# Optimization experiments

Hardware: AMD Instinct MI355X
Metric: run time of the kernel (lower is better)

## Reference

```python
import jax, jax.numpy as jnp
import numpy as np

B, D, H = 4096, 256, 1024
TRACE_STEPS = 10
T_FINAL = 1.0


def setup_inputs() -> dict:
    key = jax.random.key(0)
    k0, k1, k2 = jax.random.split(key, 3)
    s1 = 1.0 / np.sqrt(D + 1)
    s2 = 1.0 / np.sqrt(H)
    return {
        "x": jax.random.normal(k0, (B, D), dtype=jnp.float32),
        "W1": jax.random.uniform(k1, (D + 1, H), jnp.float32, -s1, s1),
        "b1": jnp.zeros((H,), jnp.float32),
        "W2": jax.random.uniform(k2, (H, D), jnp.float32, -s2, s2),
        "b2": jnp.zeros((D,), jnp.float32),
    }


def _odefun(params, t, z):
    # FFJORD vector field: tanh MLP on [z, t]. z: [B, D] -> [B, D]
    W1, b1, W2, b2 = params
    tcol = jnp.full((z.shape[0], 1), t, dtype=z.dtype)
    h = jnp.tanh(jnp.concatenate([z, tcol], axis=-1) @ W1 + b1)
    return h @ W2 + b2


def _rademacher(key, shape, dtype):
    # randint(0,2)*2-1, matching the torch probe construction
    return jax.random.randint(key, shape, 0, 2).astype(dtype) * 2.0 - 1.0


def _aug_dynamics(params, t, state, e):
    # state: [B, D+1] = [z | logp]; e: [TRACE_STEPS, B, D] Rademacher probes.
    # torch computes etf = grad((f*e).sum(), z) = e^T J, div = (e^T J)*e summed.
    # e^T J e == e . (J e), so forward-mode jvp gives identical math.
    z = state[:, :-1]
    f = lambda zz: _odefun(params, t, zz)

    def probe(ei):
        f_z, Je = jax.jvp(f, (z,), (ei,))
        return f_z, jnp.sum(Je * ei, axis=-1)  # [B]

    f_z, divs = jax.vmap(probe)(e)
    f_z = f_z[0]                       # primal identical across probes
    div_est = jnp.mean(divs, axis=0)   # average of trace_steps estimates
    return jnp.concatenate([f_z, -div_est[:, None]], axis=-1)


def reference(x, W1, b1, W2, b2):
    params = (W1, b1, W2, b2)
    Bx = x.shape[0]
    ekey = jax.random.key(42)
    probes = lambda i: _rademacher(jax.random.fold_in(ekey, i), (TRACE_STEPS, Bx, D), x.dtype)

    # initial augmented state: [z, logp=0]
    y0 = jnp.concatenate([x, jnp.zeros((Bx, 1), x.dtype)], axis=-1)

    # t_grid = [0, T] with 2 points -> fixed-grid rk4 takes ONE RK4 step of size T
    h = T_FINAL
    g = lambda t, y, i: _aug_dynamics(params, t, y, probes(i))
    k1 = g(0.0, y0, 0)
    k2 = g(0.5 * h, y0 + 0.5 * h * k1, 1)
    k3 = g(0.5 * h, y0 + 0.5 * h * k2, 2)
    k4 = g(h, y0 + h * k3, 3)
    y1 = y0 + (h / 6.0) * (k1 + 2.0 * k2 + 2.0 * k3 + k4)

    # module returns the full trajectory `output`: [len(t_grid), B, D+1]
    return jnp.stack([y0, y1], axis=0)
```

## Files before the change

### kernel.cpp

```cpp
#include <hip/hip_runtime.h>
#include <stdint.h>

#define BATCH 4096
#define DIMD  256
#define DIMH  1024
#define EPAD  264
#define NEPW  163840

typedef __attribute__((ext_vector_type(8))) short short8;
typedef __attribute__((ext_vector_type(4))) float float4v;

struct Keys4 { uint32_t a[4]; uint32_t b[4]; };

__host__ __device__ static inline uint32_t rotl32(uint32_t v, int r) {
    return (v << r) | (v >> (32 - r));
}

__host__ __device__ static inline void tf2x32(uint32_t k0, uint32_t k1,
                                              uint32_t c0, uint32_t c1,
                                              uint32_t& o0, uint32_t& o1) {
    uint32_t ks0 = k0, ks1 = k1, ks2 = k0 ^ k1 ^ 0x1BD11BDAu;
    uint32_t x0 = c0 + ks0, x1 = c1 + ks1;
#define TF_R4(a, b, c, d)                                   \
    x0 += x1; x1 = rotl32(x1, a); x1 ^= x0;                 \
    x0 += x1; x1 = rotl32(x1, b); x1 ^= x0;                 \
    x0 += x1; x1 = rotl32(x1, c); x1 ^= x0;                 \
    x0 += x1; x1 = rotl32(x1, d); x1 ^= x0;
    TF_R4(13, 15, 26, 6)  x0 += ks1; x1 += ks2 + 1u;
    TF_R4(17, 29, 16, 24) x0 += ks2; x1 += ks0 + 2u;
    TF_R4(13, 15, 26, 6)  x0 += ks0; x1 += ks1 + 3u;
    TF_R4(17, 29, 16, 24) x0 += ks1; x1 += ks2 + 4u;
    TF_R4(13, 15, 26, 6)  x0 += ks2; x1 += ks0 + 5u;
#undef TF_R4
    o0 = x0; o1 = x1;
}

__device__ static inline short f2bf(float f) {
    uint32_t u = __float_as_uint(f);
    uint32_t r = (u + 0x7FFFu + ((u >> 16) & 1u)) >> 16;
    return (short)r;
}

__global__ __launch_bounds__(256) void k_prep(
    const float* __restrict__ x,  const float* __restrict__ W1,
    const float* __restrict__ W2, short* __restrict__ W1T,
    short* __restrict__ W2B, short* __restrict__ W2T,
    short* __restrict__ zb, float* __restrict__ dv)
{
    const int idx = blockIdx.x * 256 + threadIdx.x;
    if (idx < 262144) {
        const int n = idx >> 8, d = idx & 255;
        W1T[idx] = f2bf(W1[d * DIMH + n]);
    } else if (idx < 524288) {
        const int i = idx - 262144;
        W2B[i] = f2bf(W2[i]);
    } else if (idx < 786432) {
        const int i = idx - 524288;
        const int d = i >> 10, k = i & 1023;
        W2T[i] = f2bf(W2[k * DIMD + d]);
    } else if (idx < 1835008) {
        const int i = idx - 786432;
        zb[i] = f2bf(x[i]);
    } else if (idx < 1851392) {
        dv[idx - 1835008] = 0.0f;
    }
}

__global__ __launch_bounds__(256) void k_egen4(
    uint64_t* __restrict__ Ep, Keys4 keys)
{
    const int s = blockIdx.y;
    const uint32_t j = blockIdx.x * 256 + threadIdx.x;
    uint32_t y0, y1;
    tf2x32(keys.a[s], keys.b[s], 0u, j, y0, y1);
    uint64_t mask = __ballot(((y0 ^ y1) & 1u) != 0u);
    if ((threadIdx.x & 63) == 0)
        Ep[(size_t)s * NEPW + (j >> 6)] = mask;
}

__global__ __launch_bounds__(256) void k_pre_div(
    const short* __restrict__ Zb, const short* __restrict__ W1T,
    const short* __restrict__ W2B, const float* __restrict__ W1,
    const float* __restrict__ b1, float tval,
    const uint64_t* __restrict__ Ep, short* __restrict__ h_bf,
    float* __restrict__ divacc)
{
    __shared__ short E[64 * EPAD];
    const int t = threadIdx.x;
    const int nt = blockIdx.x;
    const int b0 = blockIdx.y * 64;
    const int wave = t >> 6, lane = t & 63;
    const int col = lane & 15, kq = lane >> 4;
    const int n = nt * 64 + wave * 16 + col;

    short8 bufr[8];
#pragma unroll
    for (int ks = 0; ks < 8; ++ks)
        bufr[ks] = *(const short8*)&W1T[n * DIMD + ks * 32 + kq * 8];

    float sreg[4][4];
    const float add = tval * W1[DIMD * DIMH + n] + b1[n];
#pragma unroll
    for (int ms = 0; ms < 4; ++ms) {
        float4v acc = {0.f, 0.f, 0.f, 0.f};
#pragma unroll
        for (int ks = 0; ks < 8; ++ks) {
            short8 af = *(const short8*)&Zb[(b0 + ms * 16 + col) * DIMD + ks * 32 + kq * 8];
            acc = __builtin_amdgcn_mfma_f32_16x16x32_bf16(af, bufr[ks], acc, 0, 0, 0);
        }
#pragma unroll
        for (int r = 0; r < 4; ++r) {
            float hv = tanhf(acc[r] + add);
            h_bf[(b0 + ms * 16 + kq * 4 + r) * DIMH + n] = f2bf(hv);
            sreg[ms][r] = 1.0f - hv * hv;
        }
    }

    short8 bvfr[8];
#pragma unroll
    for (int ks = 0; ks < 8; ++ks)
        bvfr[ks] = *(const short8*)&W2B[n * DIMD + ks * 32 + kq * 8];

    float rowacc[4][4];
#pragma unroll
    for (int a = 0; a < 4; ++a)
#pragma unroll
        for (int r = 0; r < 4; ++r) rowacc[a][r] = 0.0f;

    const int erow = t & 63, ecg = t >> 6;
    short* const edst = &E[erow * EPAD + ecg * 64];
    const uint64_t* const esrc = Ep + (size_t)b0 * 4 + erow * 4 + ecg;

#pragma unroll 1
    for (int probe = 0; probe < 10; ++probe) {
        __syncthreads();
        uint64_t w = esrc[(size_t)probe * BATCH * 4];
#pragma unroll
        for (int i = 0; i < 8; ++i) {
            short8 val;
#pragma unroll
            for (int k = 0; k < 8; ++k)
                val[k] = ((w >> (i * 8 + k)) & 1ull) ? (short)0x3F80 : (short)0xBF80u;
            *(short8*)&edst[i * 8] = val;
        }
        __syncthreads();

#pragma unroll
        for (int ms = 0; ms < 4; ++ms) {
            const short* arow = &E[(ms * 16 + col) * EPAD + kq * 8];
            float4v u = {0.f, 0.f, 0.f, 0.f}, v = {0.f, 0.f, 0.f, 0.f};
#pragma unroll
            for (int ks = 0; ks < 8; ++ks) {
                short8 af = *(const short8*)&arow[ks * 32];
                u = __builtin_amdgcn_mfma_f32_16x16x32_bf16(af, bufr[ks], u, 0, 0, 0);
                v = __builtin_amdgcn_mfma_f32_16x16x32_bf16(af, bvfr[ks], v, 0, 0, 0);
            }
#pragma unroll
            for (int r = 0; r < 4; ++r)
                rowacc[ms][r] += u[r] * sreg[ms][r] * v[r];
        }
    }

#pragma unroll
    for (int ms = 0; ms < 4; ++ms) {
#pragma unroll
        for (int r = 0; r < 4; ++r) {
            float p = rowacc[ms][r];
            p += __shfl_xor(p, 1, 64);
            p += __shfl_xor(p, 2, 64);
            p += __shfl_xor(p, 4, 64);
            p += __shfl_xor(p, 8, 64);
            rowacc[ms][r] = p;
        }
    }
    if (col == 0) {
#pragma unroll
        for (int ms = 0; ms < 4; ++ms)
#pragma unroll
            for (int r = 0; r < 4; ++r)
                atomicAdd(&divacc[b0 + ms * 16 + kq * 4 + r], rowacc[ms][r] * 0.1f);
    }
}

__global__ __launch_bounds__(256) void k_fz2(
    const short* __restrict__ Hb, const short* __restrict__ W2T,
    const float* __restrict__ b2, const float* __restrict__ x,
    float* __restrict__ fz, float cnext, int write_zb, short* __restrict__ zb)
{
    const int t = threadIdx.x;
    const int wave = t >> 6, lane = t & 63;
    const int col = lane & 15, kq = lane >> 4;
    const int m0 = blockIdx.x * 16;
    const int n0 = wave * 64;

    float4v acc[4];
#pragma unroll
    for (int ns = 0; ns < 4; ++ns) acc[ns] = (float4v){0.f, 0.f, 0.f, 0.f};

    const short* ap = &Hb[(m0 + col) * DIMH + kq * 8];
    short8 a_cur = *(const short8*)ap;
    short8 b_cur[4];
#pragma unroll
    for (int ns = 0; ns < 4; ++ns)
        b_cur[ns] = *(const short8*)&W2T[(n0 + ns * 16 + col) * DIMH + kq * 8];

    for (int ks = 0; ks < 31; ++ks) {
        short8 a_nxt = *(const short8*)&ap[(ks + 1) * 32];
        short8 b_nxt[4];
#pragma unroll
        for (int ns = 0; ns < 4; ++ns)
            b_nxt[ns] = *(const short8*)&W2T[(n0 + ns * 16 + col) * DIMH + (ks + 1) * 32 + kq * 8];
#pragma unroll
        for (int ns = 0; ns < 4; ++ns)
            acc[ns] = __builtin_amdgcn_mfma_f32_16x16x32_bf16(a_cur, b_cur[ns], acc[ns], 0, 0, 0);
        a_cur = a_nxt;
#pragma unroll
        for (int ns = 0; ns < 4; ++ns) b_cur[ns] = b_nxt[ns];
    }
#pragma unroll
    for (int ns = 0; ns < 4; ++ns)
        acc[ns] = __builtin_amdgcn_mfma_f32_16x16x32_bf16(a_cur, b_cur[ns], acc[ns], 0, 0, 0);

#pragma unroll
    for (int ns = 0; ns < 4; ++ns) {
        const int n = n0 + ns * 16 + col;
        const float bias = b2[n];
#pragma unroll
        for (int r = 0; r < 4; ++r) {
            const int m = m0 + kq * 4 + r;
            const float val = acc[ns][r] + bias;
            fz[m * DIMD + n] = val;
            if (write_zb)
                zb[m * DIMD + n] = f2bf(x[m * DIMD + n] + cnext * val);
        }
    }
}

__global__ __launch_bounds__(256) void k_out(
    const float* __restrict__ x, const float* __restrict__ fz,
    const float* __restrict__ divacc, float* __restrict__ out)
{
    const int idx = blockIdx.x * 256 + threadIdx.x;
    const int TOT = BATCH * (DIMD + 1);
    if (idx >= TOT) return;
    const int b = idx / (DIMD + 1);
    const int c = idx - b * (DIMD + 1);
    const float sixth = 1.0f / 6.0f;
    if (c < DIMD) {
        float xv = x[b * DIMD + c];
        int o = b * DIMD + c;
        float f1 = fz[o];
        float f2 = fz[BATCH * DIMD + o];
        float f3 = fz[2 * BATCH * DIMD + o];
        float f4 = fz[3 * BATCH * DIMD + o];
        out[idx] = xv;
        out[TOT + idx] = xv + (f1 + 2.0f * f2 + 2.0f * f3 + f4) * sixth;
    } else {
        float d1 = divacc[b];
        float d2 = divacc[BATCH + b];
        float d3 = divacc[2 * BATCH + b];
        float d4 = divacc[3 * BATCH + b];
        out[idx] = 0.0f;
        out[TOT + idx] = -(d1 + 2.0f * d2 + 2.0f * d3 + d4) * sixth;
    }
}

extern "C" void kernel_launch(void* const* d_in, const int* in_sizes, int n_in,
                              void* d_out, int out_size, void* d_ws, size_t ws_size,
                              hipStream_t stream) {
    const float* x  = (const float*)d_in[0];
    const float* W1 = (const float*)d_in[1];
    const float* b1 = (const float*)d_in[2];
    const float* W2 = (const float*)d_in[3];
    const float* b2 = (const float*)d_in[4];
    float* out = (float*)d_out;

    char* ws = (char*)d_ws;
    short* hb    = (short*)(ws);
    float* fz    = (float*)(ws + 8388608);
    short* zb    = (short*)(ws + 25165824);
    short* w1t   = (short*)(ws + 27262976);
    short* w2b   = (short*)(ws + 27787264);
    short* w2t   = (short*)(ws + 28311552);
    float* dv    = (float*)(ws + 28835840);
    uint64_t* ep = (uint64_t*)(ws + 28901376);

    Keys4 keys;
    for (uint32_t i = 0; i < 4; ++i) {
        uint32_t f0, f1, g0, g1;
        tf2x32(0u, 42u, 0u, i, f0, f1);
        tf2x32(f0, f1, 0u, 1u, g0, g1);
        keys.a[i] = g0;
        keys.b[i] = g1;
    }

    k_prep<<<7232, 256, 0, stream>>>(x, W1, W2, w1t, w2b, w2t, zb, dv);
    k_egen4<<<dim3(40960, 4), 256, 0, stream>>>(ep, keys);

    const float tvals[4] = {0.0f, 0.5f, 0.5f, 1.0f};
    const float cnext[4] = {0.5f, 0.5f, 1.0f, 0.0f};
    for (int s = 0; s < 4; ++s) {
        k_pre_div<<<dim3(16, 64), 256, 0, stream>>>(
            zb, w1t, w2b, W1, b1, tvals[s], ep + (size_t)s * NEPW,
            hb, dv + (size_t)s * BATCH);
        k_fz2<<<256, 256, 0, stream>>>(hb, w2t, b2, x,
                                       fz + (size_t)s * BATCH * DIMD,
                                       cnext[s], (s < 3) ? 1 : 0, zb);
    }
    int tot = BATCH * (DIMD + 1);
    k_out<<<(tot + 255) / 256, 256, 0, stream>>>(x, fz, dv, out);
}
```

Measured before the change: 523.9 us.

## Fuse probe generation into prep and pre-div kernels, use alignbit rotate

```diff
diff --git a/kernel.cpp b/kernel.cpp
--- a/kernel.cpp
+++ b/kernel.cpp
@@ -13,7 +13,11 @@
 struct Keys4 { uint32_t a[4]; uint32_t b[4]; };
 
 __host__ __device__ static inline uint32_t rotl32(uint32_t v, int r) {
+#ifdef __HIP_DEVICE_COMPILE__
+    return __builtin_amdgcn_alignbit(v, v, 32 - r);
+#else
     return (v << r) | (v >> (32 - r));
+#endif
 }
 
 __host__ __device__ static inline void tf2x32(uint32_t k0, uint32_t k1,
@@ -45,7 +49,8 @@
     const float* __restrict__ x,  const float* __restrict__ W1,
     const float* __restrict__ W2, short* __restrict__ W1T,
     short* __restrict__ W2B, short* __restrict__ W2T,
-    short* __restrict__ zb, float* __restrict__ dv)
+    short* __restrict__ zb, float* __restrict__ dv,
+    uint64_t* __restrict__ Ep0, uint32_t ek0, uint32_t ek1)
 {
     const int idx = blockIdx.x * 256 + threadIdx.x;
     if (idx < 262144) {
@@ -63,19 +68,14 @@
         zb[i] = f2bf(x[i]);
     } else if (idx < 1851392) {
         dv[idx - 1835008] = 0.0f;
-    }
-}
-
-__global__ __launch_bounds__(256) void k_egen4(
-    uint64_t* __restrict__ Ep, Keys4 keys)
-{
-    const int s = blockIdx.y;
-    const uint32_t j = blockIdx.x * 256 + threadIdx.x;
-    uint32_t y0, y1;
-    tf2x32(keys.a[s], keys.b[s], 0u, j, y0, y1);
-    uint64_t mask = __ballot(((y0 ^ y1) & 1u) != 0u);
-    if ((threadIdx.x & 63) == 0)
-        Ep[(size_t)s * NEPW + (j >> 6)] = mask;
+    } else {
+        const uint32_t j = (uint32_t)(idx - 1851392);
+        uint32_t y0, y1;
+        tf2x32(ek0, ek1, 0u, j, y0, y1);
+        uint64_t mask = __ballot(((y0 ^ y1) & 1u) != 0u);
+        if ((threadIdx.x & 63) == 0)
+            Ep0[j >> 6] = mask;
+    }
 }
 
 __global__ __launch_bounds__(256) void k_pre_div(
@@ -83,7 +83,8 @@
     const short* __restrict__ W2B, const float* __restrict__ W1,
     const float* __restrict__ b1, float tval,
     const uint64_t* __restrict__ Ep, short* __restrict__ h_bf,
-    float* __restrict__ divacc)
+    float* __restrict__ divacc,
+    uint64_t* __restrict__ EpNext, uint32_t nk0, uint32_t nk1, int do_egen)
 {
     __shared__ short E[64 * EPAD];
     const int t = threadIdx.x;
@@ -113,6 +114,20 @@
             float hv = tanhf(acc[r] + add);
             h_bf[(b0 + ms * 16 + kq * 4 + r) * DIMH + n] = f2bf(hv);
             sreg[ms][r] = 1.0f - hv * hv;
+        }
+    }
+
+    if (do_egen) {
+        const uint32_t bflat = (uint32_t)(blockIdx.y * 16 + blockIdx.x);
+        const uint32_t jbase = bflat * 10240u + (uint32_t)t;
+#pragma unroll 2
+        for (int w = 0; w < 40; ++w) {
+            uint32_t j = jbase + (uint32_t)w * 256u;
+            uint32_t y0, y1;
+            tf2x32(nk0, nk1, 0u, j, y0, y1);
+            uint64_t mask = __ballot(((y0 ^ y1) & 1u) != 0u);
+            if (lane == 0)
+                EpNext[j >> 6] = mask;
         }
     }
 
@@ -294,15 +309,19 @@
         keys.b[i] = g1;
     }
 
-    k_prep<<<7232, 256, 0, stream>>>(x, W1, W2, w1t, w2b, w2t, zb, dv);
-    k_egen4<<<dim3(40960, 4), 256, 0, stream>>>(ep, keys);
+    k_prep<<<48192, 256, 0, stream>>>(x, W1, W2, w1t, w2b, w2t, zb, dv,
+                                      ep, keys.a[0], keys.b[0]);
 
     const float tvals[4] = {0.0f, 0.5f, 0.5f, 1.0f};
     const float cnext[4] = {0.5f, 0.5f, 1.0f, 0.0f};
     for (int s = 0; s < 4; ++s) {
+        const int last = (s == 3);
         k_pre_div<<<dim3(16, 64), 256, 0, stream>>>(
             zb, w1t, w2b, W1, b1, tvals[s], ep + (size_t)s * NEPW,
-            hb, dv + (size_t)s * BATCH);
+            hb, dv + (size_t)s * BATCH,
+            ep + (size_t)(s + 1) * NEPW,
+            last ? 0u : keys.a[s + 1], last ? 0u : keys.b[s + 1],
+            last ? 0 : 1);
         k_fz2<<<256, 256, 0, stream>>>(hb, w2t, b2, x,
                                        fz + (size_t)s * BATCH * DIMD,
                                        cnext[s], (s < 3) ? 1 : 0, zb);
```

Result: no change. 531.9 us (+1.5%).
